# Kernel tuning notes

Measured on AMD Instinct MI355X. Metric: run time of the kernel, lower is better.

## Reference

```python
import jax, jax.numpy as jnp
import numpy as np
from jax import lax

B, T, H, W, C = 32, 250, 28, 28, 1
CLASSES, IPC = 25, 10
UNITS = 512
MEM_CELLS = CLASSES * IPC  # 250
CELL = 64
HEADS = 4
FEAT = 2 * 2 * 32          # conv output flattened = 128
XDIM = FEAT + CLASSES      # 153
IN_LSTM = XDIM + HEADS * CELL  # 409
EPS_BN = 1e-3


def setup_inputs() -> dict:
    key = jax.random.key(0)
    ks = iter(jax.random.split(key, 40))
    s = 0.02
    d = {}
    d['images'] = jax.random.normal(next(ks), (B, T, H, W, C), jnp.float32)
    d['previous_labels'] = jax.random.randint(next(ks), (B, T), 0, CLASSES, jnp.int32)
    # conv stack
    for i, (ci, co) in enumerate([(1, 8), (8, 16), (16, 32)], start=1):
        d[f'k{i}'] = jax.random.normal(next(ks), (3, 3, ci, co), jnp.float32) * s
        d[f'cb{i}'] = jnp.zeros((co,), jnp.float32)
        d[f'g{i}'] = jnp.ones((co,), jnp.float32)
        d[f'be{i}'] = jnp.zeros((co,), jnp.float32)
        d[f'mm{i}'] = jnp.zeros((co,), jnp.float32)
        d[f'mv{i}'] = jnp.ones((co,), jnp.float32)
    # LSTM cell (keras gate order i,f,g,o)
    d['Wx'] = jax.random.normal(next(ks), (IN_LSTM, 4 * UNITS), jnp.float32) * s
    d['Wh'] = jax.random.normal(next(ks), (UNITS, 4 * UNITS), jnp.float32) * s
    d['bl'] = jnp.zeros((4 * UNITS,), jnp.float32)
    # parameters dense -> (read_heads+1)*cell_size, tanh
    d['Wp'] = jax.random.normal(next(ks), (UNITS, (HEADS + 1) * CELL), jnp.float32) * s
    d['bp'] = jnp.zeros(((HEADS + 1) * CELL,), jnp.float32)
    # output layer: Dense(units, tanh) on concat(h, read_value)
    d['Wo'] = jax.random.normal(next(ks), (UNITS + HEADS * CELL, UNITS), jnp.float32) * s
    d['bo'] = jnp.zeros((UNITS,), jnp.float32)
    # final classifier
    d['Wf'] = jax.random.normal(next(ks), (UNITS, CLASSES), jnp.float32) * s
    d['bf'] = jnp.zeros((CLASSES,), jnp.float32)
    return d


def _conv_bn_relu(x, k, cb, g, be, mm, mv):
    y = lax.conv_general_dilated(x, k, (2, 2), 'VALID',
                                 dimension_numbers=('NHWC', 'HWIO', 'NHWC')) + cb
    y = (y - mm) * g * lax.rsqrt(mv + EPS_BN) + be  # inference BN
    return jax.nn.relu(y)


def _l2n(x):
    return x * lax.rsqrt(jnp.maximum(jnp.sum(x * x, axis=-1, keepdims=True), 1e-12))


def _forward(images, previous_labels, k1, cb1, g1, be1, mm1, mv1,
             k2, cb2, g2, be2, mm2, mv2, k3, cb3, g3, be3, mm3, mv3,
             Wx, Wh, bl, Wp, bp, Wo, bo, Wf, bf):
    x = images.reshape(B * T, H, W, C)
    x = _conv_bn_relu(x, k1, cb1, g1, be1, mm1, mv1)
    x = _conv_bn_relu(x, k2, cb2, g2, be2, mm2, mv2)
    x = _conv_bn_relu(x, k3, cb3, g3, be3, mm3, mv3)
    x = x.reshape(B, T, FEAT)
    oh = jax.nn.one_hot(previous_labels, CLASSES, dtype=x.dtype)
    x = jnp.concatenate([x, oh], axis=-1)  # [B, T, XDIM]

    def step(carry, xt):
        h, c, rv, mem = carry
        inp = jnp.concatenate([xt, rv], axis=-1)
        z = inp @ Wx + h @ Wh + bl
        zi, zf, zg, zo = jnp.split(z, 4, axis=-1)
        i, f, g = jax.nn.sigmoid(zi), jax.nn.sigmoid(zf), jnp.tanh(zg)
        o = jax.nn.sigmoid(zo)
        c = f * c + i * g
        h = o * jnp.tanh(c)
        hid = jnp.tanh(h @ Wp + bp)
        wv = hid[:, :CELL]                                # write value
        keys = hid[:, CELL:].reshape(B, HEADS, CELL)
        att = jnp.einsum('brs,bms->brm', _l2n(keys), _l2n(mem))
        w = jax.nn.softmax(att, axis=-1)
        rv = jnp.einsum('brm,bms->brs', w, mem).reshape(B, HEADS * CELL)
        mem = jnp.concatenate([wv[:, None, :], mem[:, :-1]], axis=1)  # shift write
        out = jnp.tanh(jnp.concatenate([h, rv], axis=-1) @ Wo + bo)
        return (h, c, rv, mem), out

    carry0 = (jnp.zeros((B, UNITS)), jnp.zeros((B, UNITS)),
              jnp.zeros((B, HEADS * CELL)), jnp.zeros((B, MEM_CELLS, CELL)))
    _, ys = lax.scan(step, carry0, jnp.swapaxes(x, 0, 1))  # ys: [T, B, UNITS]
    rnn_out = jnp.swapaxes(ys, 0, 1)
    return jax.nn.softmax(rnn_out @ Wf + bf, axis=-1)


def reference(images, previous_labels, k1, cb1, g1, be1, mm1, mv1,
              k2, cb2, g2, be2, mm2, mv2, k3, cb3, g3, be3, mm3, mv3,
              Wx, Wh, bl, Wp, bp, Wo, bo, Wf, bf):
    return _forward(images, previous_labels, k1, cb1, g1, be1, mm1, mv1,
                    k2, cb2, g2, be2, mm2, mv2, k3, cb3, g3, be3, mm3, mv3,
                    Wx, Wh, bl, Wp, bp, Wo, bo, Wf, bf)
```

## Files before the change

### kernel.cpp

```cpp
#include <hip/hip_runtime.h>


constexpr size_t OFF_FEATP  = 0;
constexpr size_t OFF_WXI    = OFF_FEATP + (size_t)8000 * 128;
constexpr size_t OFF_WHI    = OFF_WXI + (size_t)409 * 2048;
constexpr size_t OFF_BLI    = OFF_WHI + (size_t)512 * 2048;
constexpr size_t OFF_ZP2A   = OFF_BLI + 2048;
constexpr size_t OFF_ZP2B   = OFF_ZP2A + 262144;
constexpr size_t OFF_OH2A   = OFF_ZP2B + 262144;
constexpr size_t OFF_OH2B   = OFF_OH2A + 65536;
constexpr size_t OFF_OUTPRE2= OFF_OH2B + 65536;
constexpr size_t OFF_HT2    = OFF_OUTPRE2 + 32768;
constexpr size_t OFF_HTT2   = OFF_HT2 + 65536;
constexpr size_t OFF_RVT2   = OFF_HTT2 + 65536;
constexpr size_t OFF_WVP2   = OFF_RVT2 + 32768;
constexpr size_t OFF_BAR    = OFF_WVP2 + 16384;
constexpr size_t OFF_WPT    = OFF_BAR + 4096;
constexpr size_t WS_FLOATS  = OFF_WPT + (size_t)163840;

constexpr int DYN_FLOATS = 34816;
constexpr int DYN_BYTES  = DYN_FLOATS * 4;

constexpr int COH = 0, COP = 512, CCO = 1024, CRING = 1536;

__device__ __forceinline__ float sigm(float x) { return 1.f / (1.f + __expf(-x)); }

typedef int iv2 __attribute__((ext_vector_type(2)));
typedef int iv4 __attribute__((ext_vector_type(4)));
typedef float fv4 __attribute__((ext_vector_type(4)));

__device__ __forceinline__ void st_pair(float* base, size_t pidx, float v, int tag) {
  unsigned long long u = (unsigned long long)__float_as_uint(v) |
                         ((unsigned long long)(unsigned)tag << 32);
  __hip_atomic_store((unsigned long long*)(base + 2 * pidx), u,
                     __ATOMIC_RELAXED, __HIP_MEMORY_SCOPE_AGENT);
}
__device__ __forceinline__ float spin_pair(const float* base, size_t pidx, int tag) {
  const iv2* p = (const iv2*)(base + 2 * pidx);
  iv2 v;
  for (;;) {
    asm volatile("global_load_dwordx2 %0, %1, off sc0 sc1\n\ts_waitcnt vmcnt(0)"
                 : "=&v"(v) : "v"(p) : "memory");
    if (v[1] == tag) break;
    __builtin_amdgcn_s_sleep(1);
  }
  return __int_as_float(v[0]);
}
__device__ __forceinline__ float2 spin_pair_2addr(const float* a, const float* b, int tag) {
  const iv2* pa = (const iv2*)a;
  const iv2* pb = (const iv2*)b;
  iv2 x, y;
  for (;;) {
    asm volatile(
        "global_load_dwordx2 %0, %2, off sc0 sc1\n\t"
        "global_load_dwordx2 %1, %3, off sc0 sc1\n\t"
        "s_waitcnt vmcnt(0)"
        : "=&v"(x), "=&v"(y) : "v"(pa), "v"(pb) : "memory");
    if (x[1] == tag && y[1] == tag) break;
    __builtin_amdgcn_s_sleep(1);
  }
  return {__int_as_float(x[0]), __int_as_float(y[0])};
}
__device__ __forceinline__ void ld4x2_sc(const iv2* a, const iv2* b, const iv2* c,
                                         const iv2* d, iv2& x, iv2& y, iv2& z, iv2& w) {
  asm volatile(
      "global_load_dwordx2 %0, %4, off sc0 sc1\n\t"
      "global_load_dwordx2 %1, %5, off sc0 sc1\n\t"
      "global_load_dwordx2 %2, %6, off sc0 sc1\n\t"
      "global_load_dwordx2 %3, %7, off sc0 sc1\n\t"
      "s_waitcnt vmcnt(0)"
      : "=&v"(x), "=&v"(y), "=&v"(z), "=&v"(w)
      : "v"(a), "v"(b), "v"(c), "v"(d) : "memory");
}
__device__ __forceinline__ void ld8i4_sc(const iv4* b0, iv4* v) {
  const iv4 *p0 = b0, *p1 = b0 + 512, *p2 = b0 + 1024, *p3 = b0 + 1536,
            *p4 = b0 + 2048, *p5 = b0 + 2560, *p6 = b0 + 3072, *p7 = b0 + 3584;
  asm volatile(
      "global_load_dwordx4 %0, %8, off sc0 sc1\n\t"
      "global_load_dwordx4 %1, %9, off sc0 sc1\n\t"
      "global_load_dwordx4 %2, %10, off sc0 sc1\n\t"
      "global_load_dwordx4 %3, %11, off sc0 sc1\n\t"
      "global_load_dwordx4 %4, %12, off sc0 sc1\n\t"
      "global_load_dwordx4 %5, %13, off sc0 sc1\n\t"
      "global_load_dwordx4 %6, %14, off sc0 sc1\n\t"
      "global_load_dwordx4 %7, %15, off sc0 sc1\n\t"
      "s_waitcnt vmcnt(0)"
      : "=&v"(v[0]), "=&v"(v[1]), "=&v"(v[2]), "=&v"(v[3]),
        "=&v"(v[4]), "=&v"(v[5]), "=&v"(v[6]), "=&v"(v[7])
      : "v"(p0), "v"(p1), "v"(p2), "v"(p3), "v"(p4), "v"(p5), "v"(p6), "v"(p7)
      : "memory");
}
__device__ __forceinline__ void ld10i4_sc(const iv4* b0, const iv4* z0,
                                          const iv4* z1, iv4* v) {
  const iv4 *p0 = b0, *p1 = b0 + 512, *p2 = b0 + 1024, *p3 = b0 + 1536,
            *p4 = b0 + 2048, *p5 = b0 + 2560, *p6 = b0 + 3072, *p7 = b0 + 3584;
  asm volatile(
      "global_load_dwordx4 %0, %10, off sc0 sc1\n\t"
      "global_load_dwordx4 %1, %11, off sc0 sc1\n\t"
      "global_load_dwordx4 %2, %12, off sc0 sc1\n\t"
      "global_load_dwordx4 %3, %13, off sc0 sc1\n\t"
      "global_load_dwordx4 %4, %14, off sc0 sc1\n\t"
      "global_load_dwordx4 %5, %15, off sc0 sc1\n\t"
      "global_load_dwordx4 %6, %16, off sc0 sc1\n\t"
      "global_load_dwordx4 %7, %17, off sc0 sc1\n\t"
      "global_load_dwordx4 %8, %18, off sc0 sc1\n\t"
      "global_load_dwordx4 %9, %19, off sc0 sc1\n\t"
      "s_waitcnt vmcnt(0)"
      : "=&v"(v[0]), "=&v"(v[1]), "=&v"(v[2]), "=&v"(v[3]), "=&v"(v[4]),
        "=&v"(v[5]), "=&v"(v[6]), "=&v"(v[7]), "=&v"(v[8]), "=&v"(v[9])
      : "v"(p0), "v"(p1), "v"(p2), "v"(p3), "v"(p4), "v"(p5), "v"(p6), "v"(p7),
        "v"(z0), "v"(z1)
      : "memory");
}
__device__ __forceinline__ int sum8_bar(const int* b) {
  int v0, v1, v2, v3, v4, v5, v6, v7;
  asm volatile(
      "global_load_dword %0, %8, off sc0 sc1\n\t"
      "global_load_dword %1, %9, off sc0 sc1\n\t"
      "global_load_dword %2, %10, off sc0 sc1\n\t"
      "global_load_dword %3, %11, off sc0 sc1\n\t"
      "global_load_dword %4, %12, off sc0 sc1\n\t"
      "global_load_dword %5, %13, off sc0 sc1\n\t"
      "global_load_dword %6, %14, off sc0 sc1\n\t"
      "global_load_dword %7, %15, off sc0 sc1\n\t"
      "s_waitcnt vmcnt(0)"
      : "=&v"(v0), "=&v"(v1), "=&v"(v2), "=&v"(v3),
        "=&v"(v4), "=&v"(v5), "=&v"(v6), "=&v"(v7)
      : "v"(b), "v"(b + 64), "v"(b + 128), "v"(b + 192),
        "v"(b + 256), "v"(b + 320), "v"(b + 384), "v"(b + 448)
      : "memory");
  return ((v0 + v1) + (v2 + v3)) + ((v4 + v5) + (v6 + v7));
}

__global__ __launch_bounds__(256) void prep_kernel(const float* __restrict__ Wx,
                                                   const float* __restrict__ Wh,
                                                   const float* __restrict__ bl,
                                                   const float* __restrict__ Wp,
                                                   float* __restrict__ ws) {
  float* WXI = ws + OFF_WXI;
  float* WHI = ws + OFF_WHI;
  float* BLI = ws + OFF_BLI;
  float* WPT = ws + OFF_WPT;
  const int t0 = 409 * 2048;
  const int t1 = t0 + 512 * 2048;
  const int t2 = t1 + 2048;
  const int total = t2 + 163840;
  for (int idx = blockIdx.x * blockDim.x + threadIdx.x; idx < total;
       idx += gridDim.x * blockDim.x) {
    if (idx < t0) {
      int k = idx >> 11, cc = idx & 2047;
      WXI[idx] = Wx[(size_t)k * 2048 + (cc & 3) * 512 + (cc >> 2)];
    } else if (idx < t1) {
      int j = idx - t0;
      int k = j >> 11, cc = j & 2047;
      WHI[j] = Wh[(size_t)k * 2048 + (cc & 3) * 512 + (cc >> 2)];
    } else if (idx < t2) {
      int cc = idx - t1;
      BLI[cc] = bl[(cc & 3) * 512 + (cc >> 2)];
    } else {
      int e = idx - t2;
      int k4 = e / 1280, r = e - k4 * 1280;
      int j = r >> 2, ks = r & 3;
      WPT[e] = Wp[(size_t)(k4 * 4 + ks) * 320 + j];
    }
  }
}

__global__ __launch_bounds__(128) void conv_kernel(
    const float* __restrict__ img,
    const float* __restrict__ k1, const float* __restrict__ cb1, const float* __restrict__ g1,
    const float* __restrict__ be1, const float* __restrict__ mm1, const float* __restrict__ mv1,
    const float* __restrict__ k2, const float* __restrict__ cb2, const float* __restrict__ g2,
    const float* __restrict__ be2, const float* __restrict__ mm2, const float* __restrict__ mv2,
    const float* __restrict__ k3, const float* __restrict__ cb3, const float* __restrict__ g3,
    const float* __restrict__ be3, const float* __restrict__ mm3, const float* __restrict__ mv3,
    float* __restrict__ ws) {
  __shared__ float s_in[784];
  __shared__ float s_y1[13 * 13 * 8];
  __shared__ float s_y2[6 * 6 * 16];
  __shared__ float s_k1[72], s_k2[1152], s_k3[4608];
  __shared__ float s_s1[8], s_b1[8], s_s2[16], s_b2[16], s_s3[32], s_b3[32];
  float* FEATP = ws + OFF_FEATP;
  const int n = blockIdx.x, tid = threadIdx.x;
  const float* ip = img + (size_t)n * 784;
  for (int i = tid; i < 784; i += 128) s_in[i] = ip[i];
  for (int i = tid; i < 72; i += 128) s_k1[i] = k1[i];
  for (int i = tid; i < 1152; i += 128) s_k2[i] = k2[i];
  for (int i = tid; i < 4608; i += 128) s_k3[i] = k3[i];
  if (tid < 8) {
    float s = g1[tid] * rsqrtf(mv1[tid] + 1e-3f);
    s_s1[tid] = s; s_b1[tid] = (cb1[tid] - mm1[tid]) * s + be1[tid];
  } else if (tid >= 32 && tid < 48) {
    int c = tid - 32;
    float s = g2[c] * rsqrtf(mv2[c] + 1e-3f);
    s_s2[c] = s; s_b2[c] = (cb2[c] - mm2[c]) * s + be2[c];
  } else if (tid >= 64 && tid < 96) {
    int c = tid - 64;
    float s = g3[c] * rsqrtf(mv3[c] + 1e-3f);
    s_s3[c] = s; s_b3[c] = (cb3[c] - mm3[c]) * s + be3[c];
  }
  __syncthreads();
  for (int idx = tid; idx < 13 * 13 * 8; idx += 128) {
    int co = idx & 7, pos = idx >> 3;
    int j = pos % 13, i = pos / 13;
    float acc = 0.f;
    #pragma unroll
    for (int ky = 0; ky < 3; ++ky)
      #pragma unroll
      for (int kx = 0; kx < 3; ++kx)
        acc += s_in[(2 * i + ky) * 28 + (2 * j + kx)] * s_k1[(ky * 3 + kx) * 8 + co];
    float v = acc * s_s1[co] + s_b1[co];
    s_y1[idx] = v > 0.f ? v : 0.f;
  }
  __syncthreads();
  for (int idx = tid; idx < 6 * 6 * 16; idx += 128) {
    int co = idx & 15, pos = idx >> 4;
    int j = pos % 6, i = pos / 6;
    float acc = 0.f;
    for (int ky = 0; ky < 3; ++ky)
      for (int kx = 0; kx < 3; ++kx) {
        int base = ((2 * i + ky) * 13 + (2 * j + kx)) * 8;
        int kb = (ky * 3 + kx) * 128 + co;
        #pragma unroll
        for (int ci = 0; ci < 8; ++ci) acc += s_y1[base + ci] * s_k2[kb + ci * 16];
      }
    float v = acc * s_s2[co] + s_b2[co];
    s_y2[idx] = v > 0.f ? v : 0.f;
  }
  __syncthreads();
  for (int idx = tid; idx < 128; idx += 128) {
    int co = idx & 31, pos = idx >> 5;
    int j = pos & 1, i = pos >> 1;
    float acc = 0.f;
    for (int ky = 0; ky < 3; ++ky)
      for (int kx = 0; kx < 3; ++kx) {
        int base = ((2 * i + ky) * 6 + (2 * j + kx)) * 16;
        int kb = (ky * 3 + kx) * 512 + co;
        #pragma unroll
        for (int ci = 0; ci < 16; ++ci) acc += s_y2[base + ci] * s_k3[kb + ci * 32];
      }
    float v = acc * s_s3[co] + s_b3[co];
    FEATP[(size_t)n * 128 + idx] = v > 0.f ? v : 0.f;
  }
}

__global__ __launch_bounds__(512) void lstm_kernel(
    const int* __restrict__ labels,
    const float* __restrict__ Wo, const float* __restrict__ bo,
    const float* __restrict__ Wp, const float* __restrict__ bp,
    const float* __restrict__ Wf, const float* __restrict__ bf,
    float* __restrict__ ws, float* __restrict__ out) {
  extern __shared__ float dyn[];
  const float* FEATP = ws + OFF_FEATP;
  const float* WXI   = ws + OFF_WXI;
  const float* WHI   = ws + OFF_WHI;
  const float* BLI   = ws + OFF_BLI;
  float* ZP2A   = ws + OFF_ZP2A;
  float* ZP2B   = ws + OFF_ZP2B;
  float* OH2A   = ws + OFF_OH2A;
  float* OH2B   = ws + OFF_OH2B;
  float* OUTPRE2= ws + OFF_OUTPRE2;
  float* HT2    = ws + OFF_HT2;
  float* HTT2   = ws + OFF_HTT2;
  float* RVT2   = ws + OFF_RVT2;
  float* WVP2   = ws + OFF_WVP2;
  const float* WPT = ws + OFF_WPT;
  int*   BARp   = (int*)(ws + OFF_BAR);

  const int bid = blockIdx.x;
  const int tid = threadIdx.x;

  int* bc = (int*)(dyn + 34808);
  auto waitC = [&](int base, int target, int& cache) {
    if (cache >= target) return;
    if (tid == 0) {
      int v = sum8_bar(BARp + base);
      while (v < target) v = sum8_bar(BARp + base);
      bc[base >> 9] = v;
    }
    __syncthreads();
    cache = bc[base >> 9];
    __syncthreads();
  };
  auto bumpC = [&](int base) {
    asm volatile("s_waitcnt vmcnt(0)" ::: "memory");
    __syncthreads();
    if (tid == 0) atomicAdd(&BARp[base + ((bid & 7) << 6)], 1);
  };

  auto stageP = [&](float* dst, const float* srcPairs, int tag) {
    const iv4* sp = (const iv4*)srcPairs + tid;
    iv4 v[8];
    for (;;) {
      ld8i4_sc(sp, v);
      bool ok = true;
      #pragma unroll
      for (int j = 0; j < 8; ++j) ok = ok && (v[j][1] == tag) && (v[j][3] == tag);
      if (ok) break;
      __builtin_amdgcn_s_sleep(2);
    }
    #pragma unroll
    for (int j = 0; j < 8; ++j) {
      int i = (tid + j * 512) << 1;
      float2 f = {__int_as_float(v[j][0]), __int_as_float(v[j][2])};
      *(float2*)&dst[(i >> 5) * 36 + (i & 31)] = f;
    }
  };

  auto E32 = [&](const float* Wm, const float* Am, int K, float* part, float2& r) {
    const int wv = tid >> 6, l = tid & 63;
    const int ksub = l & 1, cg = (l >> 1) & 3, bg = l >> 3;
    const int Kp = K >> 4;
    const int kb = wv * (K >> 3) + ksub * Kp;
    const float* wp = Wm + (size_t)kb * 32 + cg * 8;
    const float* ap = Am + (size_t)kb * 36 + bg * 4;
    float4 acc[8];
    #pragma unroll
    for (int i = 0; i < 8; ++i) acc[i] = {0.f, 0.f, 0.f, 0.f};
    #pragma unroll 4
    for (int kk = 0; kk < Kp; ++kk) {
      float4 w0 = *(const float4*)(wp + kk * 32);
      float4 w1 = *(const float4*)(wp + kk * 32 + 4);
      float4 a  = *(const float4*)(ap + kk * 36);
      float wl[8];
      *(float4*)&wl[0] = w0; *(float4*)&wl[4] = w1;
      #pragma unroll
      for (int i = 0; i < 8; ++i) {
        acc[i].x = fmaf(wl[i], a.x, acc[i].x);
        acc[i].y = fmaf(wl[i], a.y, acc[i].y);
        acc[i].z = fmaf(wl[i], a.z, acc[i].z);
        acc[i].w = fmaf(wl[i], a.w, acc[i].w);
      }
    }
    #pragma unroll
    for (int i = 0; i < 8; ++i) {
      acc[i].x += __shfl_xor(acc[i].x, 1, 64);
      acc[i].y += __shfl_xor(acc[i].y, 1, 64);
      acc[i].z += __shfl_xor(acc[i].z, 1, 64);
      acc[i].w += __shfl_xor(acc[i].w, 1, 64);
    }
    const int ob = (cg * 8) * 36 + bg * 4;
    if (ksub == 0 && wv < 4) {
      float* pb = part + wv * 1152 + ob;
      #pragma unroll
      for (int i = 0; i < 8; ++i) *(float4*)(pb + i * 36) = acc[i];
    }
    __syncthreads();
    if (ksub == 0 && wv >= 4) {
      float* pb = part + (wv - 4) * 1152 + ob;
      #pragma unroll
      for (int i = 0; i < 8; ++i) {
        float4 t = *(float4*)(pb + i * 36);
        t.x += acc[i].x; t.y += acc[i].y; t.z += acc[i].z; t.w += acc[i].w;
        *(float4*)(pb + i * 36) = t;
      }
    }
    __syncthreads();
    const int c = tid & 31, b2 = (tid >> 5) * 2;
    const int o = c * 36 + b2;
    float2 s0 = *(float2*)(part + o);
    float2 s1 = *(float2*)(part + 1152 + o);
    float2 s2 = *(float2*)(part + 2304 + o);
    float2 s3 = *(float2*)(part + 3456 + o);
    r.x = (s0.x + s1.x) + (s2.x + s3.x);
    r.y = (s0.y + s1.y) + (s2.y + s3.y);
  };

  auto E64 = [&](const float* Wm, const float* Am, float* part, float4& r) {
    const int wv = tid >> 6, l = tid & 63;
    const int ksub = l & 1, cg = (l >> 1) & 7, bg = l >> 4;
    const int kb = wv * 32 + ksub * 16;
    const float* wp0 = Wm + (size_t)kb * 64 + ((cg * 8 + ksub * 4) & 63);
    const float* wp1 = Wm + (size_t)kb * 64 + ((cg * 8 + 4 + ksub * 4) & 63);
    const float* ap = Am + (size_t)kb * 36 + bg * 8;
    float4 acc[8][2];
    #pragma unroll
    for (int i = 0; i < 8; ++i) { acc[i][0] = {0.f,0.f,0.f,0.f}; acc[i][1] = {0.f,0.f,0.f,0.f}; }
    #pragma unroll 2
    for (int kk = 0; kk < 16; ++kk) {
      float4 w0 = *(const float4*)(wp0 + kk * 64);
      float4 w1 = *(const float4*)(wp1 + kk * 64);
      float4 a0 = *(const float4*)(ap + kk * 36);
      float4 a1 = *(const float4*)(ap + kk * 36 + 4);
      float wl[8];
      *(float4*)&wl[0] = w0; *(float4*)&wl[4] = w1;
      #pragma unroll
      for (int i = 0; i < 8; ++i) {
        acc[i][0].x = fmaf(wl[i], a0.x, acc[i][0].x);
        acc[i][0].y = fmaf(wl[i], a0.y, acc[i][0].y);
        acc[i][0].z = fmaf(wl[i], a0.z, acc[i][0].z);
        acc[i][0].w = fmaf(wl[i], a0.w, acc[i][0].w);
        acc[i][1].x = fmaf(wl[i], a1.x, acc[i][1].x);
        acc[i][1].y = fmaf(wl[i], a1.y, acc[i][1].y);
        acc[i][1].z = fmaf(wl[i], a1.z, acc[i][1].z);
        acc[i][1].w = fmaf(wl[i], a1.w, acc[i][1].w);
      }
    }
    #pragma unroll
    for (int i = 0; i < 8; ++i) {
      #pragma unroll
      for (int j = 0; j < 2; ++j) {
        acc[i][j].x += __shfl_xor(acc[i][j].x, 1, 64);
        acc[i][j].y += __shfl_xor(acc[i][j].y, 1, 64);
        acc[i][j].z += __shfl_xor(acc[i][j].z, 1, 64);
        acc[i][j].w += __shfl_xor(acc[i][j].w, 1, 64);
      }
    }
    const int ob = (cg * 8) * 36 + bg * 8;
    if (ksub == 0 && wv < 4) {
      float* pb = part + wv * 2304 + ob;
      #pragma unroll
      for (int i = 0; i < 8; ++i) {
        *(float4*)(pb + i * 36) = acc[i][0];
        *(float4*)(pb + i * 36 + 4) = acc[i][1];
      }
    }
    __syncthreads();
    if (ksub == 0 && wv >= 4) {
      float* pb = part + (wv - 4) * 2304 + ob;
      #pragma unroll
      for (int i = 0; i < 8; ++i) {
        float4 t0 = *(float4*)(pb + i * 36);
        float4 t1 = *(float4*)(pb + i * 36 + 4);
        t0.x += acc[i][0].x; t0.y += acc[i][0].y; t0.z += acc[i][0].z; t0.w += acc[i][0].w;
        t1.x += acc[i][1].x; t1.y += acc[i][1].y; t1.z += acc[i][1].z; t1.w += acc[i][1].w;
        *(float4*)(pb + i * 36) = t0;
        *(float4*)(pb + i * 36 + 4) = t1;
      }
    }
    __syncthreads();
    const int c = tid & 63, b4 = (tid >> 6) * 4;
    const int o = c * 36 + b4;
    float4 s0 = *(float4*)(part + o);
    float4 s1 = *(float4*)(part + 2304 + o);
    float4 s2 = *(float4*)(part + 4608 + o);
    float4 s3 = *(float4*)(part + 6912 + o);
    r.x = (s0.x + s1.x) + (s2.x + s3.x);
    r.y = (s0.y + s1.y) + (s2.y + s3.y);
    r.z = (s0.z + s1.z) + (s2.z + s3.z);
    r.w = (s0.w + s1.w) + (s2.w + s3.w);
  };

  if (bid < 64) {
    const int c0 = bid * 32;
    for (int i = tid; i < 8192; i += 512)
      dyn[i] = WXI[(size_t)(153 + (i >> 5)) * 2048 + c0 + (i & 31)];
    for (int i = tid; i < 4096; i += 512)
      dyn[8192 + i] = WXI[(size_t)(i >> 5) * 2048 + c0 + (i & 31)];
    if (tid < 256) dyn[12288 + tid] = 0.f;
  } else if (bid < 80) {
    const int u0 = (bid - 64) * 32;
    for (int i = tid; i < 8192; i += 512)
      dyn[i] = Wo[(size_t)(512 + (i >> 5)) * 512 + u0 + (i & 31)];
    if (tid < 32) dyn[8192 + tid] = bo[u0 + tid];
  } else if (bid < 144) {
    const int r = bid - 80;
    const int j0 = (r & 31) * 64, kh = r >> 5;
    for (int i = tid; i < 16384; i += 512) {
      int k = i >> 6, cc = i & 63;
      int cr = (cc + ((k >> 4) & 1) * 4) & 63;
      dyn[k * 64 + cr] = WHI[(size_t)(kh * 256 + k) * 2048 + j0 + cc];
    }
  } else if (bid < 160) {
    const int u0 = (bid - 144) * 32;
    for (int i = tid; i < 8192; i += 512)
      dyn[i] = Wo[(size_t)(i >> 5) * 512 + u0 + (i & 31)];
  } else if (bid < 176) {
    const int u0 = (bid - 160) * 32;
    for (int i = tid; i < 8192; i += 512)
      dyn[i] = Wo[(size_t)(256 + (i >> 5)) * 512 + u0 + (i & 31)];
  } else if (bid < 240) {
    const int hp = (bid - 176) & 1;
    for (int i = tid; i < 17000; i += 512) dyn[i] = 0.f;
    if (tid < 256) dyn[17000 + tid] = rsqrtf(1e-12f);
    if (tid < 128) dyn[21264 + tid] = bp[64 + hp * 128 + tid];
    if (tid < 64)  dyn[21392 + tid] = bp[tid];
  } else if (bid < 244) {
    const int kh = (bid - 240) >> 1, cp = (bid - 240) & 1;
    for (int i = tid; i < 8192; i += 512) {
      int k = i >> 5, c = i & 31;
      dyn[i] = Wp[(size_t)(kh * 256 + k) * 320 + cp * 32 + c];
    }
  } else if (bid < 252) {
    for (int i = tid; i < 12800; i += 512) dyn[i] = Wf[i];
    if (tid < 25) dyn[12800 + tid] = bf[tid];
  }
  __syncthreads();

  auto azStage = [&](int t) {
    const float* rvP = RVT2 + ((t + 1) & 1) * 16384;
    const float* zaP = ZP2A + (t & 1) * 131072;
    const float* zbP = ZP2B + (t & 1) * 131072;
    float* rvT = dyn + 12544; float* zf = dyn + 27392;
    const int bb = tid >> 4, c2 = tid & 15;
    const iv4* rp = (const iv4*)rvP + tid;
    const size_t zi = (size_t)bb * 1024 + bid * 16 + c2;
    const iv4* za = (const iv4*)zaP + zi;
    const iv4* zb = (const iv4*)zbP + zi;
    iv4 v[10];
    for (;;) {
      ld10i4_sc(rp, za, zb, v);
      bool ok = true;
      #pragma unroll
      for (int j = 0; j < 8; ++j) ok = ok && (v[j][1] == t) && (v[j][3] == t);
      ok = ok && (v[8][1] == t + 1) && (v[8][3] == t + 1) &&
                 (v[9][1] == t + 1) && (v[9][3] == t + 1);
      if (ok) break;
      __builtin_amdgcn_s_sleep(1);
    }
    #pragma unroll
    for (int j = 0; j < 8; ++j) {
      int i = (tid + j * 512) << 1;
      float2 f = {__int_as_float(v[j][0]), __int_as_float(v[j][2])};
      *(float2*)&rvT[(i >> 5) * 36 + (i & 31)] = f;
    }
    float2 s = {__int_as_float(v[8][0]) + __int_as_float(v[9][0]),
                __int_as_float(v[8][2]) + __int_as_float(v[9][2])};
    *(float2*)&zf[bb * 32 + c2 * 2] = s;
  };
  auto azX = [&](int tt) {
    float* Wxx = dyn + 8192; float* xT = dyn + 21760;
    float* zx = dyn + 26368; float* part = dyn + 28416;
    for (int i = tid; i < 4096; i += 512) {
      int b = i >> 7, k = i & 127;
      xT[k * 36 + b] = FEATP[((size_t)b * 250 + tt) * 128 + k];
    }
    __syncthreads();
    float2 r;
    E32(Wxx, xT, 128, part, r);
    const int c = tid & 31, b2 = (tid >> 5) * 2;
    zx[b2 * 32 + c] = r.x;
    zx[(b2 + 1) * 32 + c] = r.y;
  };
  auto aoOut = [&](int t) {
    const int u0 = (bid - 64) * 32;
    const float* rvP  = RVT2 + ((t + 1) & 1) * 16384;
    const float* ohaP = OH2A + ((t + 1) & 1) * 32768;
    const float* ohbP = OH2B + ((t + 1) & 1) * 32768;
    float* W = dyn; float* bo_l = dyn + 8192; float* rvT = dyn + 8224;
    float* of = dyn + 17440; float* part = dyn + 18464;
    {
      const int b = tid >> 4, c2 = tid & 15;
      const iv4* rp = (const iv4*)rvP + tid;
      const iv4* za = (const iv4*)ohaP + (b * 256 + (u0 >> 1) + c2);
      const iv4* zb = (const iv4*)ohbP + (b * 256 + (u0 >> 1) + c2);
      iv4 v[10];
      for (;;) {
        ld10i4_sc(rp, za, zb, v);
        bool ok = true;
        #pragma unroll
        for (int j = 0; j < 10; ++j) ok = ok && (v[j][1] == t) && (v[j][3] == t);
        if (ok) break;
        __builtin_amdgcn_s_sleep(2);
      }
      #pragma unroll
      for (int j = 0; j < 8; ++j) {
        int i = (tid + j * 512) << 1;
        float2 f = {__int_as_float(v[j][0]), __int_as_float(v[j][2])};
        *(float2*)&rvT[(i >> 5) * 36 + (i & 31)] = f;
      }
      float2 s = {__int_as_float(v[8][0]) + __int_as_float(v[9][0]),
                  __int_as_float(v[8][2]) + __int_as_float(v[9][2])};
      *(float2*)&of[b * 32 + c2 * 2] = s;
    }
    __syncthreads();
    float2 r;
    E32(W, rvT, 256, part, r);
    const int c = tid & 31, b2 = (tid >> 5) * 2;
    float bv = bo_l[c];
    st_pair(OUTPRE2, (size_t)b2 * 512 + u0 + c, r.x + of[b2 * 32 + c] + bv, t);
    st_pair(OUTPRE2, (size_t)(b2 + 1) * 512 + u0 + c, r.y + of[(b2 + 1) * 32 + c] + bv, t);
  };
  auto p2Gemm = [&](int t) {
    const float* htP = HT2 + (t & 1) * 32768;
    float* W = dyn; float* A = dyn + 8192; float* part = dyn + 17408;
    const bool isOLr = bid < 160;
    stageP(A, isOLr ? htP : (htP + 16384), t + 1);
    __syncthreads();
    float2 r;
    E32(W, A, 256, part, r);
    const int c = tid & 31, b2 = (tid >> 5) * 2;
    const int u0 = (isOLr ? (bid - 144) : (bid - 160)) * 32;
    float* d = (isOLr ? OH2A : OH2B) + (t & 1) * 32768;
    st_pair(d, (size_t)b2 * 512 + u0 + c, r.x, t + 1);
    st_pair(d, (size_t)(b2 + 1) * 512 + u0 + c, r.y, t + 1);
  };

  if (bid < 64) {
    int cCOH = 0;
    float* Wz = dyn; float* Cst = dyn + 12288; float* rvT = dyn + 12544;
    float* zx = dyn + 26368; float* zf = dyn + 27392; float* part = dyn + 28416;
    azX(0);
    for (int t = 0; t < 250; ++t) {
      azStage(t);
      if (t >= 2) waitC(COH, 32 * (t - 1), cCOH);
      __syncthreads();
      float2 r;
      E32(Wz, rvT, 256, part, r);
      const int c = tid & 31, b2 = (tid >> 5) * 2;
      zf[b2 * 32 + c] += r.x + zx[b2 * 32 + c];
      zf[(b2 + 1) * 32 + c] += r.y + zx[(b2 + 1) * 32 + c];
      __syncthreads();
      if (tid < 256) {
        int u = tid & 7, b = tid >> 3;
        float4 z = *(float4*)(zf + b * 32 + u * 4);
        float ig = sigm(z.x), fg = sigm(z.y), gg = tanhf(z.z), og = sigm(z.w);
        float cc = fg * Cst[b * 8 + u] + ig * gg;
        Cst[b * 8 + u] = cc;
        float hv = og * tanhf(cc);
        st_pair(HT2 + (t & 1) * 32768, (size_t)(bid * 8 + u) * 32 + b, hv, t + 1);
        st_pair(HTT2 + (t & 1) * 32768, (size_t)b * 512 + bid * 8 + u, hv, t + 1);
      }
      if (t < 249) azX(t + 1);
    }
  } else if (bid < 80) {
    int cCCO = 0;
    for (int t = 1; t <= 250; ++t) {
      if (t >= 2) waitC(CCO, 8 * (t - 1), cCCO);
      aoOut(t);
      bumpC(COP);
    }
  } else if (bid < 144) {
    const int r = bid - 80;
    const int j0 = (r & 31) * 64, kh = r >> 5;
    const int c = tid & 63, b4 = (tid >> 6) * 4;
    float* W = dyn; float* A = dyn + 16384; float* part = dyn + 25600;
    float* zpBase = kh ? ZP2B : ZP2A;
    const float blv = (kh == 0) ? BLI[j0 + c] : 0.f;
    for (int s = 0; s < 250; ++s) {
      float wx0 = 0.f, wx1 = 0.f, wx2 = 0.f, wx3 = 0.f;
      if (kh == 0) {
        int l0 = labels[(b4 + 0) * 250 + s], l1 = labels[(b4 + 1) * 250 + s];
        int l2 = labels[(b4 + 2) * 250 + s], l3 = labels[(b4 + 3) * 250 + s];
        wx0 = WXI[(size_t)(128 + l0) * 2048 + j0 + c];
        wx1 = WXI[(size_t)(128 + l1) * 2048 + j0 + c];
        wx2 = WXI[(size_t)(128 + l2) * 2048 + j0 + c];
        wx3 = WXI[(size_t)(128 + l3) * 2048 + j0 + c];
      }
      stageP(A, HT2 + ((s + 1) & 1) * 32768 + kh * 16384, s);
      __syncthreads();
      float4 rr;
      E64(W, A, part, rr);
      float* zpD = zpBase + (s & 1) * 131072;
      st_pair(zpD, (size_t)(b4 + 0) * 2048 + j0 + c, rr.x + blv + wx0, s + 1);
      st_pair(zpD, (size_t)(b4 + 1) * 2048 + j0 + c, rr.y + blv + wx1, s + 1);
      st_pair(zpD, (size_t)(b4 + 2) * 2048 + j0 + c, rr.z + blv + wx2, s + 1);
      st_pair(zpD, (size_t)(b4 + 3) * 2048 + j0 + c, rr.w + blv + wx3, s + 1);
    }
  } else if (bid < 176) {
    int cCOP = 0;
    for (int t = 0; t < 250; ++t) {
      if (t >= 2) waitC(COP, 16 * (t - 1), cCOP);
      p2Gemm(t);
      bumpC(COH);
    }
  } else if (bid < 240) {
    float* ring = dyn;
    float* rn   = dyn + 17000;
    float* h_s  = dyn + 17256;
    float* kpart= dyn + 17768;
    float* kn   = dyn + 18408;
    float* att  = dyn + 18536;
    float* redS = dyn + 19068;
    float* pslab= dyn + 19088;
    float* bpk  = dyn + 21264;
    float* bpw  = dyn + 21392;
    const int b = (bid - 176) >> 1, hp = (bid - 176) & 1;
    const int j = tid & 127, q = tid >> 7;
    const int J = 64 + hp * 128 + j;
    const fv4* wbase = (const fv4*)WPT + q * 32 * 320 + J;
    int cCOP = 0;
    for (int t = 0; t < 250; ++t) {
      fv4 pf[16];
      #pragma unroll
      for (int i = 0; i < 16; ++i) pf[i] = wbase[i * 320];
      asm volatile("" :: "v"(pf[0]), "v"(pf[1]), "v"(pf[2]), "v"(pf[3]),
                         "v"(pf[4]), "v"(pf[5]), "v"(pf[6]), "v"(pf[7]),
                         "v"(pf[8]), "v"(pf[9]), "v"(pf[10]), "v"(pf[11]),
                         "v"(pf[12]), "v"(pf[13]), "v"(pf[14]), "v"(pf[15]));
      if (t >= 2) waitC(COP, 16 * (t - 1), cCOP);
      h_s[tid] = spin_pair(HTT2 + (t & 1) * 32768, (size_t)b * 512 + tid, t + 1);
      __syncthreads();
      {
        float a = 0.f;
        #pragma unroll
        for (int i = 0; i < 16; ++i) {
          fv4 h4 = *(const fv4*)&h_s[q * 128 + i * 4];
          a += pf[i].x * h4.x + pf[i].y * h4.y + pf[i].z * h4.z + pf[i].w * h4.w;
        }
        #pragma unroll 4
        for (int i = 16; i < 32; ++i) {
          fv4 w4 = wbase[i * 320];
          fv4 h4 = *(const fv4*)&h_s[q * 128 + i * 4];
          a += w4.x * h4.x + w4.y * h4.y + w4.z * h4.z + w4.w * h4.w;
        }
        kpart[q * 128 + j] = a;
      }
      __syncthreads();
      if (tid < 128) {
        float kr = kpart[tid] + kpart[128 + tid] + kpart[256 + tid] +
                   kpart[384 + tid] + bpk[tid];
        float v = tanhf(kr);
        float pq = v * v;
        #pragma unroll
        for (int off = 32; off; off >>= 1) pq += __shfl_xor(pq, off, 64);
        kn[tid] = v * rsqrtf(fmaxf(pq, 1e-12f));
      }
      __syncthreads();
      const int start = 250 - t;
      const int m = tid >> 1, hh = tid & 1;
      {
        float e = 0.f;
        if (m < t) {
          const float4* c4 = (const float4*)ring + (start + m) * 17;
          const float4* k4 = (const float4*)kn + hh * 16;
          float d = 0.f;
          #pragma unroll
          for (int s4 = 0; s4 < 16; ++s4) {
            float4 cc = c4[s4], kk = k4[s4];
            d += cc.x * kk.x + cc.y * kk.y + cc.z * kk.z + cc.w * kk.w;
          }
          e = __expf(d * rn[start + m]);
          att[hh * 256 + m] = e;
        } else if (m < 250) {
          e = 1.f;
        }
        float sm = e;
        #pragma unroll
        for (int off = 2; off <= 32; off <<= 1) sm += __shfl_xor(sm, off, 64);
        if ((tid & 63) < 2) redS[(tid >> 6) * 2 + (tid & 1)] = sm;
      }
      __syncthreads();
      {
        int hh2 = tid >> 8, s4 = (tid >> 4) & 15, g = tid & 15;
        float4 a4 = {0.f, 0.f, 0.f, 0.f};
        for (int mm = g; mm < t; mm += 16) {
          float w = att[hh2 * 256 + mm];
          float4 cc = ((const float4*)ring)[(start + mm) * 17 + s4];
          a4.x = fmaf(w, cc.x, a4.x); a4.y = fmaf(w, cc.y, a4.y);
          a4.z = fmaf(w, cc.z, a4.z); a4.w = fmaf(w, cc.w, a4.w);
        }
        *(float4*)&pslab[(hh2 * 16 + s4) * 68 + g * 4] = a4;
      }
      __syncthreads();
      if (tid < 128) {
        int hh3 = tid >> 6, s = tid & 63;
        float denom = redS[hh3];
        #pragma unroll
        for (int w = 1; w < 8; ++w) denom += redS[w * 2 + hh3];
        float sum = 0.f;
        #pragma unroll
        for (int g = 0; g < 16; ++g)
          sum += pslab[(hh3 * 16 + (s >> 2)) * 68 + g * 4 + (s & 3)];
        st_pair(RVT2 + (t & 1) * 16384,
                (size_t)((2 * hp + hh3) * 64 + s) * 32 + b, sum / denom, t + 1);
      }
      __syncthreads();
      {
        const int ip = 249 - t;
        if (tid < 64) {
          float2 p01 = spin_pair_2addr(
              WVP2 + (t & 1) * 8192 + 2 * ((size_t)b * 64 + tid),
              WVP2 + (t & 1) * 8192 + 4096 + 2 * ((size_t)b * 64 + tid), t + 1);
          float nv = tanhf(p01.x + p01.y + bpw[tid]);
          ring[ip * 68 + tid] = nv;
          float n2 = nv * nv;
          #pragma unroll
          for (int off = 32; off; off >>= 1) n2 += __shfl_xor(n2, off, 64);
          if (tid == 0) rn[ip] = rsqrtf(fmaxf(n2, 1e-12f));
        }
      }
      bumpC(CRING);
    }
  } else if (bid < 244) {
    const int kh = (bid - 240) >> 1, cp = (bid - 240) & 1;
    float* W = dyn; float* A = dyn + 8192; float* part = dyn + 17408;
    int cCR = 0;
    for (int t = 0; t < 250; ++t) {
      if (t >= 2) waitC(CRING, 64 * (t - 1), cCR);
      stageP(A, HT2 + (t & 1) * 32768 + kh * 16384, t + 1);
      __syncthreads();
      float2 r;
      E32(W, A, 256, part, r);
      const int c = tid & 31, b2 = (tid >> 5) * 2;
      float* d = WVP2 + (t & 1) * 8192 + kh * 4096;
      st_pair(d, (size_t)b2 * 64 + cp * 32 + c, r.x, t + 1);
      st_pair(d, (size_t)(b2 + 1) * 64 + cp * 32 + c, r.y, t + 1);
    }
  } else if (bid < 252) {
    const int b0 = (bid - 244) * 4;
    float* WfL = dyn; float* bfL = dyn + 12800;
    float* to4 = dyn + 12832;
    float* lp  = dyn + 14880;
    float* lg  = dyn + 15280;
    for (int t = 1; t <= 250; ++t) {
      {
        const iv2* p0 = (const iv2*)(OUTPRE2 + 2 * ((size_t)(b0 + 0) * 512 + tid));
        const iv2* p1 = (const iv2*)(OUTPRE2 + 2 * ((size_t)(b0 + 1) * 512 + tid));
        const iv2* p2 = (const iv2*)(OUTPRE2 + 2 * ((size_t)(b0 + 2) * 512 + tid));
        const iv2* p3 = (const iv2*)(OUTPRE2 + 2 * ((size_t)(b0 + 3) * 512 + tid));
        iv2 v0, v1, v2, v3;
        for (;;) {
          ld4x2_sc(p0, p1, p2, p3, v0, v1, v2, v3);
          if (v0[1] == t && v1[1] == t && v2[1] == t && v3[1] == t) break;
          __builtin_amdgcn_s_sleep(2);
        }
        to4[tid]        = tanhf(__int_as_float(v0[0]));
        to4[512 + tid]  = tanhf(__int_as_float(v1[0]));
        to4[1024 + tid] = tanhf(__int_as_float(v2[0]));
        to4[1536 + tid] = tanhf(__int_as_float(v3[0]));
      }
      __syncthreads();
      for (int i = 0; i < 4; ++i) {
        float* to = to4 + i * 512;
        if (tid < 400) {
          int l = tid % 25, p = tid / 25;
          float s = 0.f;
          #pragma unroll
          for (int q = 0; q < 32; ++q) { int k = p * 32 + q; s += to[k] * WfL[k * 25 + l]; }
          lp[p * 25 + l] = s;
        }
        __syncthreads();
        if (tid < 25) {
          float s = bfL[tid];
          #pragma unroll
          for (int p = 0; p < 16; ++p) s += lp[p * 25 + tid];
          lg[tid] = s;
        }
        __syncthreads();
        if (tid == 0) {
          float mx = lg[0];
          for (int l = 1; l < 25; ++l) mx = fmaxf(mx, lg[l]);
          float ss = 0.f;
          for (int l = 0; l < 25; ++l) ss += __expf(lg[l] - mx);
          lg[25] = mx; lg[26] = 1.f / ss;
        }
        __syncthreads();
        if (tid < 25)
          out[((size_t)(b0 + i) * 250 + (t - 1)) * 25 + tid] =
              __expf(lg[tid] - lg[25]) * lg[26];
        __syncthreads();
      }
      bumpC(CCO);
    }
  }
}

extern "C" void kernel_launch(void* const* d_in, const int* in_sizes, int n_in,
                              void* d_out, int out_size, void* d_ws, size_t ws_size,
                              hipStream_t stream) {
  const float* images = (const float*)d_in[0];
  const int* labels = (const int*)d_in[1];
  const float* k1  = (const float*)d_in[2];
  const float* cb1 = (const float*)d_in[3];
  const float* g1  = (const float*)d_in[4];
  const float* be1 = (const float*)d_in[5];
  const float* mm1 = (const float*)d_in[6];
  const float* mv1 = (const float*)d_in[7];
  const float* k2  = (const float*)d_in[8];
  const float* cb2 = (const float*)d_in[9];
  const float* g2  = (const float*)d_in[10];
  const float* be2 = (const float*)d_in[11];
  const float* mm2 = (const float*)d_in[12];
  const float* mv2 = (const float*)d_in[13];
  const float* k3  = (const float*)d_in[14];
  const float* cb3 = (const float*)d_in[15];
  const float* g3  = (const float*)d_in[16];
  const float* be3 = (const float*)d_in[17];
  const float* mm3 = (const float*)d_in[18];
  const float* mv3 = (const float*)d_in[19];
  const float* Wx  = (const float*)d_in[20];
  const float* Wh  = (const float*)d_in[21];
  const float* bl  = (const float*)d_in[22];
  const float* Wp  = (const float*)d_in[23];
  const float* bp  = (const float*)d_in[24];
  const float* Wo  = (const float*)d_in[25];
  const float* bo  = (const float*)d_in[26];
  const float* Wf  = (const float*)d_in[27];
  const float* bf  = (const float*)d_in[28];
  float* ws = (float*)d_ws;

  hipFuncSetAttribute((const void*)lstm_kernel,
                      hipFuncAttributeMaxDynamicSharedMemorySize, DYN_BYTES);

  hipMemsetAsync((char*)d_ws + OFF_ZP2A * sizeof(float), 0,
                 (OFF_WPT - OFF_ZP2A) * sizeof(float), stream);
  prep_kernel<<<1024, 256, 0, stream>>>(Wx, Wh, bl, Wp, ws);
  conv_kernel<<<8000, 128, 0, stream>>>(images,
      k1, cb1, g1, be1, mm1, mv1,
      k2, cb2, g2, be2, mm2, mv2,
      k3, cb3, g3, be3, mm3, mv3, ws);
  lstm_kernel<<<256, 512, DYN_BYTES, stream>>>(labels, Wo, bo, Wp, bp, Wf, bf, ws,
                                               (float*)d_out);
}
```

Before: 3.825 ms.

## Split memory-attention blocks into per-head waves with LDS flag sync instead of barriers

```diff
diff --git a/kernel.cpp b/kernel.cpp
--- a/kernel.cpp
+++ b/kernel.cpp
@@ -34,17 +34,6 @@
                          ((unsigned long long)(unsigned)tag << 32);
   __hip_atomic_store((unsigned long long*)(base + 2 * pidx), u,
                      __ATOMIC_RELAXED, __HIP_MEMORY_SCOPE_AGENT);
-}
-__device__ __forceinline__ float spin_pair(const float* base, size_t pidx, int tag) {
-  const iv2* p = (const iv2*)(base + 2 * pidx);
-  iv2 v;
-  for (;;) {
-    asm volatile("global_load_dwordx2 %0, %1, off sc0 sc1\n\ts_waitcnt vmcnt(0)"
-                 : "=&v"(v) : "v"(p) : "memory");
-    if (v[1] == tag) break;
-    __builtin_amdgcn_s_sleep(1);
-  }
-  return __int_as_float(v[0]);
 }
 __device__ __forceinline__ float2 spin_pair_2addr(const float* a, const float* b, int tag) {
   const iv2* pa = (const iv2*)a;
@@ -111,6 +100,16 @@
       : "v"(p0), "v"(p1), "v"(p2), "v"(p3), "v"(p4), "v"(p5), "v"(p6), "v"(p7),
         "v"(z0), "v"(z1)
       : "memory");
+}
+__device__ __forceinline__ void ld4i4o_sc(const iv4* b0, iv4& a, iv4& b,
+                                          iv4& c, iv4& d) {
+  asm volatile(
+      "global_load_dwordx4 %0, %4, off sc0 sc1\n\t"
+      "global_load_dwordx4 %1, %4, off offset:16 sc0 sc1\n\t"
+      "global_load_dwordx4 %2, %4, off offset:32 sc0 sc1\n\t"
+      "global_load_dwordx4 %3, %4, off offset:48 sc0 sc1\n\t"
+      "s_waitcnt vmcnt(0)"
+      : "=&v"(a), "=&v"(b), "=&v"(c), "=&v"(d) : "v"(b0) : "memory");
 }
 __device__ __forceinline__ int sum8_bar(const int* b) {
   int v0, v1, v2, v3, v4, v5, v6, v7;
@@ -475,6 +474,7 @@
     if (tid < 256) dyn[17000 + tid] = rsqrtf(1e-12f);
     if (tid < 128) dyn[21264 + tid] = bp[64 + hp * 128 + tid];
     if (tid < 64)  dyn[21392 + tid] = bp[tid];
+    if (tid < 4)   ((int*)(dyn + 21456))[tid] = 0;
   } else if (bid < 244) {
     const int kh = (bid - 240) >> 1, cp = (bid - 240) & 1;
     for (int i = tid; i < 8192; i += 512) {
@@ -657,120 +657,129 @@
   } else if (bid < 240) {
     float* ring = dyn;
     float* rn   = dyn + 17000;
-    float* h_s  = dyn + 17256;
-    float* kpart= dyn + 17768;
-    float* kn   = dyn + 18408;
-    float* att  = dyn + 18536;
-    float* redS = dyn + 19068;
-    float* pslab= dyn + 19088;
-    float* bpk  = dyn + 21264;
-    float* bpw  = dyn + 21392;
+    int* flags  = (int*)(dyn + 21456);
     const int b = (bid - 176) >> 1, hp = (bid - 176) & 1;
-    const int j = tid & 127, q = tid >> 7;
-    const int J = 64 + hp * 128 + j;
-    const fv4* wbase = (const fv4*)WPT + q * 32 * 320 + J;
-    int cCOP = 0;
-    for (int t = 0; t < 250; ++t) {
-      fv4 pf[16];
-      #pragma unroll
-      for (int i = 0; i < 16; ++i) pf[i] = wbase[i * 320];
-      asm volatile("" :: "v"(pf[0]), "v"(pf[1]), "v"(pf[2]), "v"(pf[3]),
-                         "v"(pf[4]), "v"(pf[5]), "v"(pf[6]), "v"(pf[7]),
-                         "v"(pf[8]), "v"(pf[9]), "v"(pf[10]), "v"(pf[11]),
-                         "v"(pf[12]), "v"(pf[13]), "v"(pf[14]), "v"(pf[15]));
-      if (t >= 2) waitC(COP, 16 * (t - 1), cCOP);
-      h_s[tid] = spin_pair(HTT2 + (t & 1) * 32768, (size_t)b * 512 + tid, t + 1);
-      __syncthreads();
-      {
-        float a = 0.f;
-        #pragma unroll
-        for (int i = 0; i < 16; ++i) {
-          fv4 h4 = *(const fv4*)&h_s[q * 128 + i * 4];
-          a += pf[i].x * h4.x + pf[i].y * h4.y + pf[i].z * h4.z + pf[i].w * h4.w;
-        }
-        #pragma unroll 4
-        for (int i = 16; i < 32; ++i) {
-          fv4 w4 = wbase[i * 320];
-          fv4 h4 = *(const fv4*)&h_s[q * 128 + i * 4];
-          a += w4.x * h4.x + w4.y * h4.y + w4.z * h4.z + w4.w * h4.w;
-        }
-        kpart[q * 128 + j] = a;
-      }
-      __syncthreads();
-      if (tid < 128) {
-        float kr = kpart[tid] + kpart[128 + tid] + kpart[256 + tid] +
-                   kpart[384 + tid] + bpk[tid];
-        float v = tanhf(kr);
-        float pq = v * v;
+    const int w = tid >> 6, l = tid & 63;
+
+    if (w < 2) {
+      float* hS   = dyn + 17256 + w * 512;
+      float* knS  = dyn + 18280 + w * 64;
+      float* attS = dyn + 18408 + w * 256;
+      const float bpkv = dyn[21264 + w * 64 + l];
+      const fv4* wb = (const fv4*)WPT + (64 + hp * 128 + w * 64 + l);
+      const int m16 = l & 15, dg = l >> 4;
+      int copC = 0;
+      for (int t = 0; t < 250; ++t) {
+        {
+          const iv4* hb = (const iv4*)(HTT2 + (t & 1) * 32768) + b * 256 + l * 4;
+          iv4 a0, a1, a2, a3;
+          for (;;) {
+            ld4i4o_sc(hb, a0, a1, a2, a3);
+            if (a0[1] == t + 1 && a0[3] == t + 1 && a1[1] == t + 1 && a1[3] == t + 1 &&
+                a2[1] == t + 1 && a2[3] == t + 1 && a3[1] == t + 1 && a3[3] == t + 1)
+              break;
+            __builtin_amdgcn_s_sleep(1);
+          }
+          float2 f;
+          f = {__int_as_float(a0[0]), __int_as_float(a0[2])}; *(float2*)&hS[l * 8 + 0] = f;
+          f = {__int_as_float(a1[0]), __int_as_float(a1[2])}; *(float2*)&hS[l * 8 + 2] = f;
+          f = {__int_as_float(a2[0]), __int_as_float(a2[2])}; *(float2*)&hS[l * 8 + 4] = f;
+          f = {__int_as_float(a3[0]), __int_as_float(a3[2])}; *(float2*)&hS[l * 8 + 6] = f;
+        }
+        asm volatile("s_waitcnt lgkmcnt(0)" ::: "memory");
+        __builtin_amdgcn_sched_barrier(0);
+        float acc = 0.f;
+        #pragma unroll 8
+        for (int k4 = 0; k4 < 128; ++k4) {
+          fv4 wv4 = wb[(size_t)k4 * 320];
+          fv4 h4 = *(const fv4*)&hS[k4 * 4];
+          acc = fmaf(wv4.x, h4.x, acc);
+          acc = fmaf(wv4.y, h4.y, acc);
+          acc = fmaf(wv4.z, h4.z, acc);
+          acc = fmaf(wv4.w, h4.w, acc);
+        }
+        float kv = tanhf(acc + bpkv);
+        float pq = kv * kv;
         #pragma unroll
         for (int off = 32; off; off >>= 1) pq += __shfl_xor(pq, off, 64);
-        kn[tid] = v * rsqrtf(fmaxf(pq, 1e-12f));
-      }
-      __syncthreads();
-      const int start = 250 - t;
-      const int m = tid >> 1, hh = tid & 1;
-      {
-        float e = 0.f;
-        if (m < t) {
-          const float4* c4 = (const float4*)ring + (start + m) * 17;
-          const float4* k4 = (const float4*)kn + hh * 16;
+        knS[l] = kv * rsqrtf(fmaxf(pq, 1e-12f));
+        asm volatile("s_waitcnt lgkmcnt(0)" ::: "memory");
+        __builtin_amdgcn_sched_barrier(0);
+        if (t >= 1) {
+          while (__hip_atomic_load(&flags[2], __ATOMIC_ACQUIRE,
+                                   __HIP_MEMORY_SCOPE_WORKGROUP) < t) {}
+          __builtin_amdgcn_sched_barrier(0);
+        }
+        const fv4 kq0 = *(const fv4*)&knS[dg * 16 + 0];
+        const fv4 kq1 = *(const fv4*)&knS[dg * 16 + 4];
+        const fv4 kq2 = *(const fv4*)&knS[dg * 16 + 8];
+        const fv4 kq3 = *(const fv4*)&knS[dg * 16 + 12];
+        const int start = 250 - t;
+        float lsum = 0.f;
+        const int jmax = (t + 15) >> 4;
+        for (int j = 0; j < jmax; ++j) {
+          int m = m16 + (j << 4);
+          bool act = m < t;
           float d = 0.f;
-          #pragma unroll
-          for (int s4 = 0; s4 < 16; ++s4) {
-            float4 cc = c4[s4], kk = k4[s4];
-            d += cc.x * kk.x + cc.y * kk.y + cc.z * kk.z + cc.w * kk.w;
+          if (act) {
+            const fv4* c4 = (const fv4*)(ring + (start + m) * 68) + dg * 4;
+            fv4 q0 = c4[0], q1 = c4[1], q2 = c4[2], q3 = c4[3];
+            d = fmaf(q0.x, kq0.x, fmaf(q0.y, kq0.y, fmaf(q0.z, kq0.z, q0.w * kq0.w)));
+            d = fmaf(q1.x, kq1.x, fmaf(q1.y, kq1.y, fmaf(q1.z, kq1.z, fmaf(q1.w, kq1.w, d))));
+            d = fmaf(q2.x, kq2.x, fmaf(q2.y, kq2.y, fmaf(q2.z, kq2.z, fmaf(q2.w, kq2.w, d))));
+            d = fmaf(q3.x, kq3.x, fmaf(q3.y, kq3.y, fmaf(q3.z, kq3.z, fmaf(q3.w, kq3.w, d))));
           }
-          e = __expf(d * rn[start + m]);
-          att[hh * 256 + m] = e;
-        } else if (m < 250) {
-          e = 1.f;
-        }
-        float sm = e;
+          d += __shfl_xor(d, 16, 64);
+          d += __shfl_xor(d, 32, 64);
+          if (act) {
+            float e = __expf(d * rn[start + m]);
+            if (dg == 0) attS[m] = e;
+            lsum += e;
+          }
+        }
         #pragma unroll
-        for (int off = 2; off <= 32; off <<= 1) sm += __shfl_xor(sm, off, 64);
-        if ((tid & 63) < 2) redS[(tid >> 6) * 2 + (tid & 1)] = sm;
-      }
-      __syncthreads();
-      {
-        int hh2 = tid >> 8, s4 = (tid >> 4) & 15, g = tid & 15;
-        float4 a4 = {0.f, 0.f, 0.f, 0.f};
-        for (int mm = g; mm < t; mm += 16) {
-          float w = att[hh2 * 256 + mm];
-          float4 cc = ((const float4*)ring)[(start + mm) * 17 + s4];
-          a4.x = fmaf(w, cc.x, a4.x); a4.y = fmaf(w, cc.y, a4.y);
-          a4.z = fmaf(w, cc.z, a4.z); a4.w = fmaf(w, cc.w, a4.w);
-        }
-        *(float4*)&pslab[(hh2 * 16 + s4) * 68 + g * 4] = a4;
-      }
-      __syncthreads();
-      if (tid < 128) {
-        int hh3 = tid >> 6, s = tid & 63;
-        float denom = redS[hh3];
+        for (int off = 8; off; off >>= 1) lsum += __shfl_xor(lsum, off, 64);
+        float denom = lsum + (float)(250 - t);
+        asm volatile("s_waitcnt lgkmcnt(0)" ::: "memory");
+        __builtin_amdgcn_sched_barrier(0);
+        const float* rb = ring + start * 68 + l;
+        float racc = 0.f;
+        int m = 0;
+        for (; m + 4 <= t; m += 4) {
+          fv4 a4 = *(const fv4*)&attS[m];
+          racc = fmaf(a4.x, rb[(m + 0) * 68], racc);
+          racc = fmaf(a4.y, rb[(m + 1) * 68], racc);
+          racc = fmaf(a4.z, rb[(m + 2) * 68], racc);
+          racc = fmaf(a4.w, rb[(m + 3) * 68], racc);
+        }
+        for (; m < t; ++m) racc = fmaf(attS[m], rb[m * 68], racc);
+        if (t >= 2 && copC < 16 * (t - 1)) {
+          do { copC = sum8_bar(BARp + COP); } while (copC < 16 * (t - 1));
+        }
+        st_pair(RVT2 + (t & 1) * 16384,
+                (size_t)((2 * hp + w) * 64 + l) * 32 + b, racc / denom, t + 1);
+      }
+    } else if (w == 2) {
+      float* bpw = dyn + 21392;
+      for (int t = 0; t < 250; ++t) {
+        float2 p01 = spin_pair_2addr(
+            WVP2 + (t & 1) * 8192 + 2 * ((size_t)b * 64 + l),
+            WVP2 + (t & 1) * 8192 + 4096 + 2 * ((size_t)b * 64 + l), t + 1);
+        float nv = tanhf(p01.x + p01.y + bpw[l]);
+        float n2 = nv * nv;
         #pragma unroll
-        for (int w = 1; w < 8; ++w) denom += redS[w * 2 + hh3];
-        float sum = 0.f;
-        #pragma unroll
-        for (int g = 0; g < 16; ++g)
-          sum += pslab[(hh3 * 16 + (s >> 2)) * 68 + g * 4 + (s & 3)];
-        st_pair(RVT2 + (t & 1) * 16384,
-                (size_t)((2 * hp + hh3) * 64 + s) * 32 + b, sum / denom, t + 1);
-      }
-      __syncthreads();
-      {
+        for (int off = 32; off; off >>= 1) n2 += __shfl_xor(n2, off, 64);
         const int ip = 249 - t;
-        if (tid < 64) {
-          float2 p01 = spin_pair_2addr(
-              WVP2 + (t & 1) * 8192 + 2 * ((size_t)b * 64 + tid),
-              WVP2 + (t & 1) * 8192 + 4096 + 2 * ((size_t)b * 64 + tid), t + 1);
-          float nv = tanhf(p01.x + p01.y + bpw[tid]);
-          ring[ip * 68 + tid] = nv;
-          float n2 = nv * nv;
-          #pragma unroll
-          for (int off = 32; off; off >>= 1) n2 += __shfl_xor(n2, off, 64);
-          if (tid == 0) rn[ip] = rsqrtf(fmaxf(n2, 1e-12f));
-        }
-      }
-      bumpC(CRING);
+        ring[ip * 68 + l] = nv;
+        if (l == 0) rn[ip] = rsqrtf(fmaxf(n2, 1e-12f));
+        asm volatile("s_waitcnt lgkmcnt(0)" ::: "memory");
+        __builtin_amdgcn_sched_barrier(0);
+        if (l == 0) {
+          __hip_atomic_store(&flags[2], t + 1, __ATOMIC_RELEASE,
+                             __HIP_MEMORY_SCOPE_WORKGROUP);
+          atomicAdd(&BARp[CRING + ((bid & 7) << 6)], 1);
+        }
+      }
     }
   } else if (bid < 244) {
     const int kh = (bid - 240) >> 1, cp = (bid - 240) & 1;
```

New measurement: 4.841 ms. +26.6%, slower.
